# Kernel optimization log

Hardware: AMD Instinct MI355X
Metric: run time of the kernel (lower is better)

Reference implementation:

```python
import jax, jax.numpy as jnp
import numpy as np

EPS = 1e-8  # torch F.cosine_similarity eps


def setup_inputs() -> dict:
    key = jax.random.key(0)
    x = jax.random.normal(key, (16, 256, 2048), dtype=jnp.float32)
    return {"x": x}


def reference(x) -> jnp.ndarray:
    # x: [b, c, p]. Pairwise cosine similarity between point columns, diag = 1.
    # Equivalent to the original O(p) loop of F.cosine_similarity calls,
    # fused into one batched matmul.
    b, c, p = x.shape
    dots = jnp.einsum("bcp,bcq->bpq", x, x)            # [b, p, p]
    norms = jnp.sqrt(jnp.sum(x * x, axis=1))            # [b, p]
    denom = jnp.maximum(norms[:, :, None] * norms[:, None, :], EPS)
    sim = dots / denom
    eye = jnp.eye(p, dtype=x.dtype)
    res = jnp.where(eye[None, :, :] > 0, jnp.ones((), x.dtype), sim)
    return res
```

## Files before the change

### kernel.cpp

```cpp
#include <hip/hip_runtime.h>

#define B_ 16
#define C_ 256
#define P_ 2048
#define BK 32
#define KT 8
#define NT 136
#define NT_OFF 120

typedef __attribute__((ext_vector_type(8))) short short8;
typedef __attribute__((ext_vector_type(4))) float floatx4;

__device__ inline short f2bf(float v) {
  union { float f; unsigned u; } c; c.f = v;
  unsigned r = c.u + 0x7fffu + ((c.u >> 16) & 1u);
  return (short)(r >> 16);
}

#define GLOAD_LDS16(g, l)                                          \
  __builtin_amdgcn_global_load_lds(                                \
      (const __attribute__((address_space(1))) void*)(g),          \
      (__attribute__((address_space(3))) void*)(l), 16, 0, 0)

__global__ __launch_bounds__(256, 4) void k_transpose(const float* __restrict__ x,
                                                      short* __restrict__ Xt,
                                                      float* __restrict__ nrm2p) {
  __shared__ float t[2][32][133];
  __shared__ float red[8][32][4];
  const int p0 = blockIdx.x * 128, b = blockIdx.y, zc = blockIdx.z;
  const float* xb = x + (size_t)b * C_ * P_;
  short* xtb = Xt + (size_t)b * P_ * C_;
  const int tid = threadIdx.x;
  const int tx = tid & 31;
  const int cg = tid >> 5;
  floatx4 s4 = (floatx4){0.f, 0.f, 0.f, 0.f};
  const int cbase = zc * 128;
#pragma unroll 1
  for (int chunk = 0; chunk < 4; ++chunk) {
    const int c0 = cbase + chunk * 32;
    const int tb = chunk & 1;
    float4 v[4];
#pragma unroll
    for (int i = 0; i < 4; ++i)
      v[i] = *reinterpret_cast<const float4*>(&xb[(size_t)(c0 + cg + i * 8) * P_ + p0 + tx * 4]);
#pragma unroll
    for (int i = 0; i < 4; ++i) {
      *reinterpret_cast<float4*>(&t[tb][cg + i * 8][tx * 4]) = v[i];
      s4[0] += v[i].x * v[i].x;
      s4[1] += v[i].y * v[i].y;
      s4[2] += v[i].z * v[i].z;
      s4[3] += v[i].w * v[i].w;
    }
    __syncthreads();
#pragma unroll
    for (int u = 0; u < 4; ++u) {
      const int unit = tid + 256 * u;
      const int r = unit >> 3, ch = unit & 7;
      short4 w;
      w.x = f2bf(t[tb][ch * 4 + 0][r]);
      w.y = f2bf(t[tb][ch * 4 + 1][r]);
      w.z = f2bf(t[tb][ch * 4 + 2][r]);
      w.w = f2bf(t[tb][ch * 4 + 3][r]);
      *reinterpret_cast<short4*>(&xtb[(size_t)(p0 + r) * C_ + c0 + ch * 4]) = w;
    }
  }
  *reinterpret_cast<floatx4*>(&red[cg][tx][0]) = s4;
  __syncthreads();
  if (tid < 128) {
    const int cgp = tid >> 2, j = tid & 3;
    float ns = 0.f;
#pragma unroll
    for (int g = 0; g < 8; ++g) ns += red[g][cgp][j];
    nrm2p[(size_t)zc * B_ * P_ + b * P_ + p0 + tid] = ns;
  }
}

__global__ __launch_bounds__(256, 4) void k_gemm(const short* __restrict__ Xt,
                                                 const float* __restrict__ nrm2p,
                                                 float* __restrict__ out) {
  const int bid = blockIdx.x;
  const int xcd = bid & 7;
  const int s = bid >> 3;
  const int b = xcd * 2 + (s >= NT);
  int t = s - (s >= NT ? NT : 0);

  int tm, tn;
  if (t < NT_OFF) {
    int rem = t, len = 15;
    tm = 0;
    while (rem >= len) { rem -= len; --len; ++tm; }
    tn = tm + 1 + rem;
  } else {
    tm = tn = t - NT_OFF;
  }
  const int p0 = tm * 128, q0 = tn * 128;
  const short* Xb = Xt + (size_t)b * P_ * C_;

  __shared__ __align__(16) char smem[32768];

  const int tid = threadIdx.x;
  const int lane = tid & 63;
  const int wid = tid >> 6;
  const int wrow = wid >> 1;
  const int wcol = wid & 1;

  floatx4 acc[4][4];
#pragma unroll
  for (int i = 0; i < 4; ++i)
#pragma unroll
    for (int j = 0; j < 4; ++j) acc[i][j] = (floatx4){0.f, 0.f, 0.f, 0.f};

  const int K2 = C_ * 2;

  auto STAGE = [&](int buf, int kt) {
    const int kb = kt * (BK * 2);
#pragma unroll
    for (int j = 0; j < 2; ++j) {
      const int chunk = j * 4 + wid;
      const int f = chunk * 1024 + lane * 16;
      const int row = f >> 6;
      const int inrow = f & 63;
      GLOAD_LDS16((const char*)Xb + (size_t)(p0 + row) * K2 + kb + inrow,
                  smem + buf * 8192 + chunk * 1024);
      GLOAD_LDS16((const char*)Xb + (size_t)(q0 + row) * K2 + kb + inrow,
                  smem + 16384 + buf * 8192 + chunk * 1024);
    }
  };

  STAGE(0, 0);

  for (int kt = 0; kt < KT; ++kt) {
    const int cur = kt & 1;
    if (kt < KT - 1) {
      STAGE(cur ^ 1, kt + 1);
      asm volatile("s_waitcnt vmcnt(4)\n\ts_barrier" ::: "memory");
    } else {
      asm volatile("s_waitcnt vmcnt(0)\n\ts_barrier" ::: "memory");
    }

    const short* As = (const short*)(smem + cur * 8192);
    const short* Bs = (const short*)(smem + 16384 + cur * 8192);
    short8 af[4], bf[4];
#pragma unroll
    for (int mi = 0; mi < 4; ++mi) {
      const int r = wrow * 64 + mi * 16 + (lane & 15);
      af[mi] = *reinterpret_cast<const short8*>(&As[r * BK + (lane >> 4) * 8]);
    }
#pragma unroll
    for (int ni = 0; ni < 4; ++ni) {
      const int r = wcol * 64 + ni * 16 + (lane & 15);
      bf[ni] = *reinterpret_cast<const short8*>(&Bs[r * BK + (lane >> 4) * 8]);
    }
#pragma unroll
    for (int mi = 0; mi < 4; ++mi)
#pragma unroll
      for (int ni = 0; ni < 4; ++ni)
        acc[mi][ni] = __builtin_amdgcn_mfma_f32_16x16x32_bf16(af[mi], bf[ni], acc[mi][ni], 0, 0, 0);

    asm volatile("s_waitcnt lgkmcnt(0)\n\ts_barrier" ::: "memory");
  }

  const float* n2a = nrm2p + (size_t)b * P_;
  const float* n2b = nrm2p + (size_t)B_ * P_ + (size_t)b * P_;
  float* ob = out + (size_t)b * P_ * P_;
  const int cl = lane & 15, rg4 = (lane >> 4) * 4;

  float rnq[4];
#pragma unroll
  for (int ni = 0; ni < 4; ++ni) {
    const int qc = q0 + wcol * 64 + ni * 16 + cl;
    rnq[ni] = __builtin_amdgcn_rcpf(fmaxf(sqrtf(n2a[qc] + n2b[qc]), 1e-4f));
  }
  floatx4 rnp[4];
#pragma unroll
  for (int mi = 0; mi < 4; ++mi) {
    const int pb = p0 + wrow * 64 + mi * 16 + rg4;
    const float4 pa = *reinterpret_cast<const float4*>(&n2a[pb]);
    const float4 pbv = *reinterpret_cast<const float4*>(&n2b[pb]);
    rnp[mi][0] = __builtin_amdgcn_rcpf(fmaxf(sqrtf(pa.x + pbv.x), 1e-4f));
    rnp[mi][1] = __builtin_amdgcn_rcpf(fmaxf(sqrtf(pa.y + pbv.y), 1e-4f));
    rnp[mi][2] = __builtin_amdgcn_rcpf(fmaxf(sqrtf(pa.z + pbv.z), 1e-4f));
    rnp[mi][3] = __builtin_amdgcn_rcpf(fmaxf(sqrtf(pa.w + pbv.w), 1e-4f));
  }

  float* etile = (float*)smem + wid * 1280;

#pragma unroll
  for (int mi = 0; mi < 4; ++mi) {
    const int prow = p0 + wrow * 64 + mi * 16 + rg4;
#pragma unroll
    for (int ni = 0; ni < 4; ++ni) {
      floatx4 vv = acc[mi][ni] * rnp[mi] * rnq[ni];
      const int qc = q0 + wcol * 64 + ni * 16 + cl;
      if (tm == tn) {
        const int d = qc - prow;
        if (d >= 0 && d < 4) vv[d] = 1.0f;
      }
      ob[(size_t)(prow + 0) * P_ + qc] = vv[0];
      ob[(size_t)(prow + 1) * P_ + qc] = vv[1];
      ob[(size_t)(prow + 2) * P_ + qc] = vv[2];
      ob[(size_t)(prow + 3) * P_ + qc] = vv[3];
      if (tm != tn)
        *reinterpret_cast<floatx4*>(&etile[(ni * 16 + cl) * 20 + rg4]) = vv;
    }
    if (tm != tn) {
      const int pcb = p0 + wrow * 64 + mi * 16;
#pragma unroll
      for (int i = 0; i < 4; ++i) {
        const int qq = i * 16 + (lane >> 2);
        const floatx4 mv = *reinterpret_cast<const floatx4*>(&etile[qq * 20 + (lane & 3) * 4]);
        *reinterpret_cast<floatx4*>(
            &ob[(size_t)(q0 + wcol * 64 + qq) * P_ + pcb + (lane & 3) * 4]) = mv;
      }
    }
  }
}

extern "C" void kernel_launch(void* const* d_in, const int* in_sizes, int n_in,
                              void* d_out, int out_size, void* d_ws, size_t ws_size,
                              hipStream_t stream) {
  const float* x = (const float*)d_in[0];
  float* out = (float*)d_out;

  short* Xt = (short*)d_ws;
  float* nrm2p = (float*)((char*)d_ws + (size_t)B_ * P_ * C_ * sizeof(short));

  k_transpose<<<dim3(P_ / 128, B_, 2), 256, 0, stream>>>(x, Xt, nrm2p);
  k_gemm<<<dim3(NT * B_), 256, 0, stream>>>(Xt, nrm2p, out);
}
```

Before: 81.79 us.

## Compute full square tile grid instead of exploiting Gram matrix symmetry

Replaces the upper-triangular tile schedule (136 tiles per batch, each off-diagonal tile also writing its mirrored transpose through LDS) with a full 16x16 tile grid where every tile computes and writes only its own block. This removes the LDS transpose staging and the strided mirrored stores, and simplifies tile index decoding. In exchange it nearly doubles the MFMA work and the operand loads per batch.

```diff
diff --git a/kernel.cpp b/kernel.cpp
--- a/kernel.cpp
+++ b/kernel.cpp
@@ -5,8 +5,6 @@
 #define P_ 2048
 #define BK 32
 #define KT 8
-#define NT 136
-#define NT_OFF 120
 
 typedef __attribute__((ext_vector_type(8))) short short8;
 typedef __attribute__((ext_vector_type(4))) float floatx4;
@@ -81,18 +79,9 @@
   const int bid = blockIdx.x;
   const int xcd = bid & 7;
   const int s = bid >> 3;
-  const int b = xcd * 2 + (s >= NT);
-  int t = s - (s >= NT ? NT : 0);
-
-  int tm, tn;
-  if (t < NT_OFF) {
-    int rem = t, len = 15;
-    tm = 0;
-    while (rem >= len) { rem -= len; --len; ++tm; }
-    tn = tm + 1 + rem;
-  } else {
-    tm = tn = t - NT_OFF;
-  }
+  const int b = xcd * 2 + (s >> 8);
+  const int t = s & 255;
+  const int tm = t >> 4, tn = t & 15;
   const int p0 = tm * 128, q0 = tn * 128;
   const short* Xb = Xt + (size_t)b * P_ * C_;
 
@@ -182,8 +171,6 @@
     rnp[mi][2] = __builtin_amdgcn_rcpf(fmaxf(sqrtf(pa.z + pbv.z), 1e-4f));
     rnp[mi][3] = __builtin_amdgcn_rcpf(fmaxf(sqrtf(pa.w + pbv.w), 1e-4f));
   }
-
-  float* etile = (float*)smem + wid * 1280;
 
 #pragma unroll
   for (int mi = 0; mi < 4; ++mi) {
@@ -200,18 +187,6 @@
       ob[(size_t)(prow + 1) * P_ + qc] = vv[1];
       ob[(size_t)(prow + 2) * P_ + qc] = vv[2];
       ob[(size_t)(prow + 3) * P_ + qc] = vv[3];
-      if (tm != tn)
-        *reinterpret_cast<floatx4*>(&etile[(ni * 16 + cl) * 20 + rg4]) = vv;
-    }
-    if (tm != tn) {
-      const int pcb = p0 + wrow * 64 + mi * 16;
-#pragma unroll
-      for (int i = 0; i < 4; ++i) {
-        const int qq = i * 16 + (lane >> 2);
-        const floatx4 mv = *reinterpret_cast<const floatx4*>(&etile[qq * 20 + (lane & 3) * 4]);
-        *reinterpret_cast<floatx4*>(
-            &ob[(size_t)(q0 + wcol * 64 + qq) * P_ + pcb + (lane & 3) * 4]) = mv;
-      }
     }
   }
 }
@@ -226,5 +201,5 @@
   float* nrm2p = (float*)((char*)d_ws + (size_t)B_ * P_ * C_ * sizeof(short));
 
   k_transpose<<<dim3(P_ / 128, B_, 2), 256, 0, stream>>>(x, Xt, nrm2p);
-  k_gemm<<<dim3(NT * B_), 256, 0, stream>>>(Xt, nrm2p, out);
-}
+  k_gemm<<<dim3(16 * 16 * B_), 256, 0, stream>>>(Xt, nrm2p, out);
+}
```

New measurement: 84.65 us. 1.04x slower.

## Give each wave private LDS staging to remove block-wide barriers in GEMM

Applied to the files above, without the earlier changes.

The shared double-buffered LDS tiles for A and B become per-wave private single buffers. Each wave loads only the 64 rows of A and 64 rows of B it consumes, so all s_barrier synchronisation in the K loop is removed and replaced by per-wave waitcnt. The next K-step's prefetch is issued after fragments are read into registers, so it overlaps the MFMAs. In exchange, rows shared between waves are fetched redundantly, roughly doubling global/L2 read traffic, and each iteration waits for its load to finish before the next one starts.

```diff
diff --git a/kernel.cpp b/kernel.cpp
--- a/kernel.cpp
+++ b/kernel.cpp
@@ -96,7 +96,7 @@
   const int p0 = tm * 128, q0 = tn * 128;
   const short* Xb = Xt + (size_t)b * P_ * C_;
 
-  __shared__ __align__(16) char smem[32768];
+  __shared__ __align__(16) short smem[4][4096];
 
   const int tid = threadIdx.x;
   const int lane = tid & 63;
@@ -104,6 +104,9 @@
   const int wrow = wid >> 1;
   const int wcol = wid & 1;
 
+  short* myA = &smem[wid][0];
+  short* myB = &smem[wid][2048];
+
   floatx4 acc[4][4];
 #pragma unroll
   for (int i = 0; i < 4; ++i)
@@ -111,53 +114,45 @@
     for (int j = 0; j < 4; ++j) acc[i][j] = (floatx4){0.f, 0.f, 0.f, 0.f};
 
   const int K2 = C_ * 2;
-
-  auto STAGE = [&](int buf, int kt) {
-    const int kb = kt * (BK * 2);
-#pragma unroll
-    for (int j = 0; j < 2; ++j) {
-      const int chunk = j * 4 + wid;
-      const int f = chunk * 1024 + lane * 16;
-      const int row = f >> 6;
-      const int inrow = f & 63;
-      GLOAD_LDS16((const char*)Xb + (size_t)(p0 + row) * K2 + kb + inrow,
-                  smem + buf * 8192 + chunk * 1024);
-      GLOAD_LDS16((const char*)Xb + (size_t)(q0 + row) * K2 + kb + inrow,
-                  smem + 16384 + buf * 8192 + chunk * 1024);
+  const int arow = (lane >> 2);
+  const int ab = (lane & 3) * 16;
+
+  auto STAGE_MY = [&](int kt) {
+    const int kb = kt * 64;
+#pragma unroll
+    for (int j = 0; j < 4; ++j) {
+      GLOAD_LDS16((const char*)Xb + (size_t)(p0 + wrow * 64 + j * 16 + arow) * K2 + kb + ab,
+                  (char*)myA + j * 1024);
+      GLOAD_LDS16((const char*)Xb + (size_t)(q0 + wcol * 64 + j * 16 + arow) * K2 + kb + ab,
+                  (char*)myB + j * 1024);
     }
   };
 
-  STAGE(0, 0);
+  STAGE_MY(0);
+  asm volatile("s_waitcnt vmcnt(0)" ::: "memory");
 
   for (int kt = 0; kt < KT; ++kt) {
-    const int cur = kt & 1;
-    if (kt < KT - 1) {
-      STAGE(cur ^ 1, kt + 1);
-      asm volatile("s_waitcnt vmcnt(4)\n\ts_barrier" ::: "memory");
-    } else {
-      asm volatile("s_waitcnt vmcnt(0)\n\ts_barrier" ::: "memory");
-    }
-
-    const short* As = (const short*)(smem + cur * 8192);
-    const short* Bs = (const short*)(smem + 16384 + cur * 8192);
     short8 af[4], bf[4];
 #pragma unroll
     for (int mi = 0; mi < 4; ++mi) {
-      const int r = wrow * 64 + mi * 16 + (lane & 15);
-      af[mi] = *reinterpret_cast<const short8*>(&As[r * BK + (lane >> 4) * 8]);
+      const int r = mi * 16 + (lane & 15);
+      af[mi] = *reinterpret_cast<const short8*>(&myA[r * BK + (lane >> 4) * 8]);
     }
 #pragma unroll
     for (int ni = 0; ni < 4; ++ni) {
-      const int r = wcol * 64 + ni * 16 + (lane & 15);
-      bf[ni] = *reinterpret_cast<const short8*>(&Bs[r * BK + (lane >> 4) * 8]);
-    }
+      const int r = ni * 16 + (lane & 15);
+      bf[ni] = *reinterpret_cast<const short8*>(&myB[r * BK + (lane >> 4) * 8]);
+    }
+    asm volatile("s_waitcnt lgkmcnt(0)" ::: "memory");
+    if (kt < KT - 1) STAGE_MY(kt + 1);
+
 #pragma unroll
     for (int mi = 0; mi < 4; ++mi)
 #pragma unroll
       for (int ni = 0; ni < 4; ++ni)
         acc[mi][ni] = __builtin_amdgcn_mfma_f32_16x16x32_bf16(af[mi], bf[ni], acc[mi][ni], 0, 0, 0);
 
-    asm volatile("s_waitcnt lgkmcnt(0)\n\ts_barrier" ::: "memory");
+    asm volatile("s_waitcnt vmcnt(0)" ::: "memory");
   }
 
   const float* n2a = nrm2p + (size_t)b * P_;
@@ -183,7 +178,7 @@
     rnp[mi][3] = __builtin_amdgcn_rcpf(fmaxf(sqrtf(pa.w + pbv.w), 1e-4f));
   }
 
-  float* etile = (float*)smem + wid * 1280;
+  float* etile = (float*)myA;
 
 #pragma unroll
   for (int mi = 0; mi < 4; ++mi) {
```

Measured after the change: 83.95 us. +2.6%, slower.
